# Kernel optimization log

Measured on AMD Instinct MI355X. Metric: run time of the kernel, lower is better.

Reference implementation:

```python
import jax, jax.numpy as jnp
import numpy as np


def setup_inputs() -> dict:
    key = jax.random.key(0)
    k1, k2 = jax.random.split(key)
    B, N, D, F = 4, 50000, 64, 100000
    verts = jax.random.normal(k1, (B, N, D), dtype=jnp.float32)
    faces = jax.random.randint(k2, (B, F, 3), 0, N, dtype=jnp.int64)
    return {"verts": verts, "faces": faces}


def reference(verts, faces):
    # verts: [B, N, D], faces: [B, F, L] int indices into N
    B, N, D = verts.shape
    Ldeg = faces.shape[-1]
    # flatten batch into one block-diagonal graph, as the torch module does
    offset = (jnp.arange(B, dtype=faces.dtype) * N)[:, None, None]
    f = (faces + offset).reshape(-1, Ldeg)          # [B*F, L]
    row = f.reshape(-1)                              # f[:, 0..L-1]
    col = jnp.roll(f, -1, axis=1).reshape(-1)        # f[:, 1..L-1, 0]
    # L = L + L.T -> edges in both directions (duplicates accumulate)
    src = jnp.concatenate([row, col])
    dst = jnp.concatenate([col, row])
    Vf = verts.reshape(-1, D)                        # [B*N, D]
    # off-diagonal: -sum_j V_j over incident half-edges (with multiplicity)
    neigh = jax.ops.segment_sum(Vf[dst], src, num_segments=B * N)
    # Lii = degree (count of incident half-edges)
    deg = jax.ops.segment_sum(jnp.ones_like(src, dtype=verts.dtype), src,
                              num_segments=B * N)    # [B*N]
    # x = (Lii * V_i - sum_j V_j) / (Lii + eps)
    x = (deg[:, None] * Vf - neigh) / (deg[:, None] + 1e-12)
    return x.reshape(B, N, D)
```

## Files before the change

### kernel.cpp

```cpp
#include <hip/hip_runtime.h>
#include <hip/hip_fp16.h>

constexpr int Bc = 4;
constexpr int Nc = 50000;
constexpr int Dc = 64;
constexpr int Fc = 100000;
constexpr int BN = Bc * Nc;
constexpr int NFACES = Bc * Fc;
constexpr int NINC = NFACES * 3;
constexpr int CAP_E = 31;

constexpr int BINV_SH = 8;
constexpr int NBINS   = (BN + 255) / 256;
constexpr int BINCAP  = 2048;
constexpr int BIN3B   = 256;
constexpr int FPB     = (NFACES + BIN3B - 1) / BIN3B;
constexpr int CONVB   = (BN * Dc / 8) / 256;
constexpr unsigned int SENT = (unsigned)Nc | ((unsigned)Nc << 16);

constexpr size_t A_VH    = 0;
constexpr size_t A_ENT   = 25600512;
constexpr size_t A_BCUR  = A_ENT + (size_t)NBINS * BINCAP * 8;
constexpr size_t A3_NEED = A_BCUR + (size_t)NBINS * 32 * 4;

__global__ __launch_bounds__(256) void bin_conv(
        const float* __restrict__ verts,
        const int*   __restrict__ faces,
        __half* __restrict__ vh,
        int*   __restrict__ bincur,
        uint2* __restrict__ entries) {
    __shared__ unsigned int sfaces[FPB * 3];
    __shared__ int scnt[NBINS];
    __shared__ int sbase[NBINS];

    if ((int)blockIdx.x < BIN3B) {
        int blk = blockIdx.x, t = threadIdx.x;
        int f0g = blk * FPB;
        int nf  = NFACES - f0g; if (nf > FPB) nf = FPB;

        for (int i = t; i < nf * 3; i += 256) sfaces[i] = (unsigned int)faces[f0g * 3 + i];
        for (int i = t; i < NBINS; i += 256) scnt[i] = 0;
        __syncthreads();

        for (int f = t; f < nf; f += 256) {
            int base = ((f0g + f) / Fc) * Nc;
            int g0 = (int)sfaces[3*f+0] + base;
            int g1 = (int)sfaces[3*f+1] + base;
            int g2 = (int)sfaces[3*f+2] + base;
            atomicAdd(&scnt[g0 >> BINV_SH], 1);
            atomicAdd(&scnt[g1 >> BINV_SH], 1);
            atomicAdd(&scnt[g2 >> BINV_SH], 1);
        }
        __syncthreads();

        for (int i = t; i < NBINS; i += 256) {
            int c = scnt[i];
            sbase[i] = (c > 0) ? atomicAdd(&bincur[i * 32], c) : 0;
            scnt[i] = 0;
        }
        __syncthreads();

        for (int f = t; f < nf; f += 256) {
            unsigned int u0 = sfaces[3*f+0];
            unsigned int u1 = sfaces[3*f+1];
            unsigned int u2 = sfaces[3*f+2];
            int base = ((f0g + f) / Fc) * Nc;
            int g0 = (int)u0 + base, g1 = (int)u1 + base, g2 = (int)u2 + base;
            int b0 = g0 >> BINV_SH, b1 = g1 >> BINV_SH, b2 = g2 >> BINV_SH;
            int p0 = sbase[b0] + atomicAdd(&scnt[b0], 1);
            if (p0 < BINCAP) entries[(size_t)b0 * BINCAP + p0] = make_uint2((unsigned)g0, u1 | (u2 << 16));
            int p1 = sbase[b1] + atomicAdd(&scnt[b1], 1);
            if (p1 < BINCAP) entries[(size_t)b1 * BINCAP + p1] = make_uint2((unsigned)g1, u0 | (u2 << 16));
            int p2 = sbase[b2] + atomicAdd(&scnt[b2], 1);
            if (p2 < BINCAP) entries[(size_t)b2 * BINCAP + p2] = make_uint2((unsigned)g2, u0 | (u1 << 16));
        }
    } else if ((int)blockIdx.x < BIN3B + CONVB) {
        long idx = ((long)(blockIdx.x - BIN3B) * 256 + threadIdx.x) * 8;
        int  v   = (int)(idx >> 6);
        int  b   = v / Nc;
        float4 a = *(const float4*)(verts + idx);
        float4 bb = *(const float4*)(verts + idx + 4);
        __half h[8];
        h[0] = __float2half(a.x);  h[1] = __float2half(a.y);
        h[2] = __float2half(a.z);  h[3] = __float2half(a.w);
        h[4] = __float2half(bb.x); h[5] = __float2half(bb.y);
        h[6] = __float2half(bb.z); h[7] = __float2half(bb.w);
        *(uint4*)(vh + idx + (long)b * 64) = *(const uint4*)h;
    } else {
        int t = threadIdx.x;
        if (t < 128) {
            int b = t >> 5, w = t & 31;
            ((unsigned int*)vh)[(long)(b * (Nc + 1) + Nc) * 32 + w] = 0u;
        }
    }
}

__global__ __launch_bounds__(256) void bucket_gather(
        const __half* __restrict__ vh,
        const uint2*  __restrict__ entries,
        const int*    __restrict__ bincur,
        float* __restrict__ out) {
    __shared__ unsigned int scnt[256];
    __shared__ unsigned int sent[256 * 32];

    int bin = blockIdx.x, t = threadIdx.x;
    scnt[t] = 0;
    for (int i = t; i < 256 * 32; i += 256) sent[i] = SENT;
    __syncthreads();

    int total = bincur[bin * 32];
    if (total > BINCAP) total = BINCAP;
    const uint2* e = entries + (size_t)bin * BINCAP;
    int v0 = bin << BINV_SH;
    for (int i = t; i < total; i += 256) {
        uint2 en = e[i];
        int vl = (int)en.x - v0;
        unsigned int r = atomicAdd(&scnt[vl], 1);
        if (r < (unsigned)CAP_E) sent[(vl << 5) + r] = en.y;
    }
    __syncthreads();

    int lane = t & 63, wv = t >> 6;
    int half = lane >> 5, j = lane & 31;
    const __half2* vh2 = (const __half2*)vh;
    int nrec = BN - v0; if (nrec > 256) nrec = 256;

    for (int pair = wv; pair * 2 < nrec; pair += 4) {
        int vl = pair * 2 + half;
        int v  = v0 + vl;
        int c  = (int)scnt[vl]; if (c > CAP_E) c = CAP_E;
        int cother = __shfl(c, lane ^ 32);
        int cmax = c > cother ? c : cother;
        int b = v / Nc;
        int base2 = b * (Nc + 1);

        float2 own = __half22float2(vh2[(v + b) * 32 + j]);

        const unsigned int* se = &sent[vl << 5];
        float accx = 0.f, accy = 0.f;
        for (int i = 0; i < cmax; i += 4) {
            unsigned int p0 = se[i];
            unsigned int p1 = se[i + 1];
            unsigned int p2 = se[i + 2];
            unsigned int p3 = se[i + 3];
            int r0 = (base2 + (int)(p0 & 0xFFFFu)) * 32 + j;
            int r1 = (base2 + (int)(p0 >> 16))     * 32 + j;
            int r2 = (base2 + (int)(p1 & 0xFFFFu)) * 32 + j;
            int r3 = (base2 + (int)(p1 >> 16))     * 32 + j;
            int r4 = (base2 + (int)(p2 & 0xFFFFu)) * 32 + j;
            int r5 = (base2 + (int)(p2 >> 16))     * 32 + j;
            int r6 = (base2 + (int)(p3 & 0xFFFFu)) * 32 + j;
            int r7 = (base2 + (int)(p3 >> 16))     * 32 + j;
            float2 f0 = __half22float2(vh2[r0]);
            float2 f1 = __half22float2(vh2[r1]);
            float2 f2 = __half22float2(vh2[r2]);
            float2 f3 = __half22float2(vh2[r3]);
            float2 f4 = __half22float2(vh2[r4]);
            float2 f5 = __half22float2(vh2[r5]);
            float2 f6 = __half22float2(vh2[r6]);
            float2 f7 = __half22float2(vh2[r7]);
            accx += (f0.x + f1.x) + (f2.x + f3.x) + (f4.x + f5.x) + (f6.x + f7.x);
            accy += (f0.y + f1.y) + (f2.y + f3.y) + (f4.y + f5.y) + (f6.y + f7.y);
        }

        float deg = 2.0f * (float)c;
        float den = deg + 1e-12f;
        float2 r;
        r.x = (deg * own.x - accx) / den;
        r.y = (deg * own.y - accy) / den;
        ((float2*)out)[(long)v * 32 + j] = r;
    }
}

constexpr size_t B_VH   = 0;
constexpr size_t B_REC  = 25600000;
constexpr size_t B_NEED = 51200000;

__global__ __launch_bounds__(256) void conv_fill(
        const float* __restrict__ verts,
        const int*   __restrict__ faces,
        __half* __restrict__ vh,
        unsigned int* __restrict__ rec) {
    constexpr int FILLB = (NFACES + 255) / 256;
    if ((int)blockIdx.x < FILLB) {
        int f = blockIdx.x * 256 + threadIdx.x;
        if (f >= NFACES) return;
        int base = (f / Fc) * Nc;
        unsigned int u0 = (unsigned int)faces[3*f+0];
        unsigned int u1 = (unsigned int)faces[3*f+1];
        unsigned int u2 = (unsigned int)faces[3*f+2];
        unsigned int* r0 = rec + (long)((int)u0 + base) * 32;
        unsigned int* r1 = rec + (long)((int)u1 + base) * 32;
        unsigned int* r2 = rec + (long)((int)u2 + base) * 32;
        int s0 = atomicAdd((int*)r0, 1);
        if (s0 < CAP_E) r0[1 + s0] = u1 | (u2 << 16);
        int s1 = atomicAdd((int*)r1, 1);
        if (s1 < CAP_E) r1[1 + s1] = u0 | (u2 << 16);
        int s2 = atomicAdd((int*)r2, 1);
        if (s2 < CAP_E) r2[1 + s2] = u0 | (u1 << 16);
    } else {
        long idx = ((long)(blockIdx.x - FILLB) * 256 + threadIdx.x) * 8;
        float4 a = *(const float4*)(verts + idx);
        float4 b = *(const float4*)(verts + idx + 4);
        __half h[8];
        h[0] = __float2half(a.x); h[1] = __float2half(a.y);
        h[2] = __float2half(a.z); h[3] = __float2half(a.w);
        h[4] = __float2half(b.x); h[5] = __float2half(b.y);
        h[6] = __float2half(b.z); h[7] = __float2half(b.w);
        *(uint4*)(vh + idx) = *(const uint4*)h;
    }
}

__global__ __launch_bounds__(256) void gather2(
        const float*  __restrict__ verts,
        const __half* __restrict__ vh,
        const unsigned int* __restrict__ rec,
        float* __restrict__ out) {
    int gtid = blockIdx.x * 256 + threadIdx.x;
    int w    = gtid >> 6;
    int lane = threadIdx.x & 63;
    int half = lane >> 5;
    int j    = lane & 31;
    int v    = 2 * w + half;
    int h32  = half << 5;

    unsigned int rw = rec[(long)w * 64 + lane];
    int c = __shfl((int)rw, h32);
    if (c > CAP_E) c = CAP_E;
    int cother = __shfl(c, lane ^ 32);
    int cmax = c > cother ? c : cother;

    int base = (v / Nc) * Nc;
    const __half2* vh2 = (const __half2*)vh;
    float2 own = ((const float2*)verts)[(long)v * 32 + j];

    float accx = 0.f, accy = 0.f;
    for (int i = 0; i < cmax; i += 2) {
        unsigned int p0 = (unsigned int)__shfl((int)rw, h32 + 1 + i);
        unsigned int p1 = (unsigned int)__shfl((int)rw, h32 + 2 + i);
        float m0 = (i < c) ? 1.f : 0.f;
        float m1 = (i + 1 < c) ? 1.f : 0.f;
        unsigned int q0 = (i < c) ? p0 : 0u;
        unsigned int q1 = (i + 1 < c) ? p1 : 0u;
        long r0 = (long)(base + (int)(q0 & 0xFFFFu)) * 32 + j;
        long r1 = (long)(base + (int)(q0 >> 16))     * 32 + j;
        long r2 = (long)(base + (int)(q1 & 0xFFFFu)) * 32 + j;
        long r3 = (long)(base + (int)(q1 >> 16))     * 32 + j;
        float2 f0 = __half22float2(vh2[r0]);
        float2 f1 = __half22float2(vh2[r1]);
        float2 f2 = __half22float2(vh2[r2]);
        float2 f3 = __half22float2(vh2[r3]);
        accx += m0 * (f0.x + f1.x) + m1 * (f2.x + f3.x);
        accy += m0 * (f0.y + f1.y) + m1 * (f2.y + f3.y);
    }

    float deg = 2.0f * (float)c;
    float den = deg + 1e-12f;
    float2 r;
    r.x = (deg * own.x - accx) / den;
    r.y = (deg * own.y - accy) / den;
    ((float2*)out)[(long)v * 32 + j] = r;
}

constexpr int SCAN_ELEMS = 1024;
constexpr int NSCAN = (BN + SCAN_ELEMS - 1) / SCAN_ELEMS;
constexpr size_t WS_COUNTS  = 0;
constexpr size_t WS_OFFSETS = 800000;
constexpr size_t WS_CURSORS = 1600000;
constexpr size_t WS_BSUMS   = 2400000;
constexpr size_t WS_BBASE   = 2401024;
constexpr size_t WS_ENTRIES = 2402048;
constexpr size_t WS_NEEDED  = WS_ENTRIES + (size_t)NINC * 8;

__global__ __launch_bounds__(256) void count_kernel(
        const int* __restrict__ faces, int* __restrict__ counts) {
    int f = blockIdx.x * blockDim.x + threadIdx.x;
    if (f >= NFACES) return;
    int base = (f / Fc) * Nc;
    atomicAdd(&counts[faces[3*f+0] + base], 1);
    atomicAdd(&counts[faces[3*f+1] + base], 1);
    atomicAdd(&counts[faces[3*f+2] + base], 1);
}

__global__ __launch_bounds__(256) void scanA(
        const int* __restrict__ counts, int* __restrict__ bsums) {
    __shared__ int s[256];
    int t = threadIdx.x, b = blockIdx.x;
    int idx = b * SCAN_ELEMS + t * 4;
    int v = 0;
    if (idx + 4 <= BN) {
        int4 c = *(const int4*)(counts + idx);
        v = c.x + c.y + c.z + c.w;
    }
    s[t] = v; __syncthreads();
    for (int o = 128; o > 0; o >>= 1) {
        if (t < o) s[t] += s[t + o];
        __syncthreads();
    }
    if (t == 0) bsums[b] = s[0];
}

__global__ __launch_bounds__(256) void scanB(
        const int* __restrict__ bsums, int* __restrict__ bbase) {
    __shared__ int s[256];
    int t = threadIdx.x;
    int x = (t < NSCAN) ? bsums[t] : 0;
    s[t] = x; __syncthreads();
    for (int o = 1; o < 256; o <<= 1) {
        int v = (t >= o) ? s[t - o] : 0;
        __syncthreads();
        s[t] += v;
        __syncthreads();
    }
    bbase[t] = s[t] - x;
}

__global__ __launch_bounds__(256) void scanC(
        const int* __restrict__ counts, const int* __restrict__ bbase,
        int* __restrict__ offsets) {
    __shared__ int s[256];
    int t = threadIdx.x, b = blockIdx.x;
    int idx = b * SCAN_ELEMS + t * 4;
    int4 c = make_int4(0, 0, 0, 0);
    bool ok = (idx + 4 <= BN);
    if (ok) c = *(const int4*)(counts + idx);
    int tsum = c.x + c.y + c.z + c.w;
    s[t] = tsum; __syncthreads();
    for (int o = 1; o < 256; o <<= 1) {
        int v = (t >= o) ? s[t - o] : 0;
        __syncthreads();
        s[t] += v;
        __syncthreads();
    }
    int tbase = bbase[b] + s[t] - tsum;
    if (ok) {
        int4 o4;
        o4.x = tbase;
        o4.y = tbase + c.x;
        o4.z = tbase + c.x + c.y;
        o4.w = tbase + c.x + c.y + c.z;
        *(int4*)(offsets + idx) = o4;
    }
}

__global__ __launch_bounds__(256) void fill_kernel(
        const int* __restrict__ faces,
        const int* __restrict__ offsets,
        int* __restrict__ cursors,
        int2* __restrict__ entries) {
    int f = blockIdx.x * blockDim.x + threadIdx.x;
    if (f >= NFACES) return;
    int base = (f / Fc) * Nc;
    int v0 = faces[3*f+0] + base;
    int v1 = faces[3*f+1] + base;
    int v2 = faces[3*f+2] + base;
    int p0 = offsets[v0] + atomicAdd(&cursors[v0], 1);
    entries[p0] = make_int2(v1, v2);
    int p1 = offsets[v1] + atomicAdd(&cursors[v1], 1);
    entries[p1] = make_int2(v0, v2);
    int p2 = offsets[v2] + atomicAdd(&cursors[v2], 1);
    entries[p2] = make_int2(v0, v1);
}

__global__ __launch_bounds__(256) void gather_kernel(
        const float* __restrict__ verts,
        const int* __restrict__ counts,
        const int* __restrict__ offsets,
        const int2* __restrict__ entries,
        float* __restrict__ out) {
    int v    = (int)((blockIdx.x * blockDim.x + threadIdx.x) >> 6);
    int lane = threadIdx.x & 63;
    if (v >= BN) return;
    int c = counts[v];
    const int2* e = entries + offsets[v];
    float acc = 0.f;
    int i = 0;
    for (; i + 2 <= c; i += 2) {
        int2 a = e[i];
        int2 b = e[i + 1];
        acc += verts[(long)a.x * Dc + lane] + verts[(long)a.y * Dc + lane]
             + verts[(long)b.x * Dc + lane] + verts[(long)b.y * Dc + lane];
    }
    if (i < c) {
        int2 a = e[i];
        acc += verts[(long)a.x * Dc + lane] + verts[(long)a.y * Dc + lane];
    }
    float deg = 2.0f * (float)c;
    float own = verts[(long)v * Dc + lane];
    out[(long)v * Dc + lane] = (deg * own - acc) / (deg + 1e-12f);
}

extern "C" void kernel_launch(void* const* d_in, const int* in_sizes, int n_in,
                              void* d_out, int out_size, void* d_ws, size_t ws_size,
                              hipStream_t stream) {
    const float* verts = (const float*)d_in[0];
    const int*   faces = (const int*)d_in[1];
    float* out = (float*)d_out;
    char*  ws  = (char*)d_ws;

    if (ws_size >= A3_NEED) {
        __half*       vh      = (__half*)(ws + A_VH);
        uint2*        entries = (uint2*)(ws + A_ENT);
        int*          bincur  = (int*)(ws + A_BCUR);

        hipMemsetAsync(bincur, 0, (size_t)NBINS * 32 * sizeof(int), stream);
        bin_conv<<<BIN3B + CONVB + 1, 256, 0, stream>>>(verts, faces, vh, bincur, entries);
        bucket_gather<<<NBINS, 256, 0, stream>>>(vh, entries, bincur, out);
    } else if (ws_size >= B_NEED) {
        __half*       vh  = (__half*)(ws + B_VH);
        unsigned int* rec = (unsigned int*)(ws + B_REC);
        hipMemsetAsync(rec, 0, (size_t)BN * 32 * sizeof(unsigned int), stream);
        conv_fill<<<(NFACES + 255) / 256 + CONVB, 256, 0, stream>>>(verts, faces, vh, rec);
        gather2<<<BN * 32 / 256, 256, 0, stream>>>(verts, vh, rec, out);
    } else if (ws_size >= WS_NEEDED) {
        int*  counts  = (int*)(ws + WS_COUNTS);
        int*  offsets = (int*)(ws + WS_OFFSETS);
        int*  cursors = (int*)(ws + WS_CURSORS);
        int*  bsums   = (int*)(ws + WS_BSUMS);
        int*  bbase   = (int*)(ws + WS_BBASE);
        int2* entries = (int2*)(ws + WS_ENTRIES);

        hipMemsetAsync(counts,  0, (size_t)BN * sizeof(int), stream);
        hipMemsetAsync(cursors, 0, (size_t)BN * sizeof(int), stream);
        int fb = (NFACES + 255) / 256;
        count_kernel<<<fb, 256, 0, stream>>>(faces, counts);
        scanA<<<NSCAN, 256, 0, stream>>>(counts, bsums);
        scanB<<<1, 256, 0, stream>>>(bsums, bbase);
        scanC<<<NSCAN, 256, 0, stream>>>(counts, bbase, offsets);
        fill_kernel<<<fb, 256, 0, stream>>>(faces, offsets, cursors, entries);
        int gb = (BN * 64 + 255) / 256;
        gather_kernel<<<gb, 256, 0, stream>>>(verts, counts, offsets, entries, out);
    }
}
```

Before: 168.0 us.

## Remap gather so each wave handles one vertex with four-way neighbor parallelism

Reworks the bucket_gather inner loop so a 64-lane wave processes one vertex. Four 16-lane groups each fetch a different neighbor row with 8-byte loads, and partial sums are then reduced across groups with xor shuffles. This replaces the two-vertices-per-wave scheme that padded to the longer neighbor list with 4-byte loads. It also vectorizes the shared-memory sentinel fill, writes float4 outputs and multiplies by a reciprocal instead of dividing. The cost is shuffle reductions and idle lanes during the final write, which only group 0 performs.

```diff
diff --git a/kernel.cpp b/kernel.cpp
--- a/kernel.cpp
+++ b/kernel.cpp
@@ -105,7 +105,11 @@
 
     int bin = blockIdx.x, t = threadIdx.x;
     scnt[t] = 0;
-    for (int i = t; i < 256 * 32; i += 256) sent[i] = SENT;
+    {
+        uint4* s4 = (uint4*)sent;
+        uint4 sv = make_uint4(SENT, SENT, SENT, SENT);
+        for (int i = t; i < 256 * 32 / 4; i += 256) s4[i] = sv;
+    }
     __syncthreads();
 
     int total = bincur[bin * 32];
@@ -121,54 +125,53 @@
     __syncthreads();
 
     int lane = t & 63, wv = t >> 6;
-    int half = lane >> 5, j = lane & 31;
-    const __half2* vh2 = (const __half2*)vh;
+    int g    = lane >> 4;
+    int j    = lane & 15;
+    int esel = g >> 1;
+    int hsel = g & 1;
     int nrec = BN - v0; if (nrec > 256) nrec = 256;
 
-    for (int pair = wv; pair * 2 < nrec; pair += 4) {
-        int vl = pair * 2 + half;
-        int v  = v0 + vl;
-        int c  = (int)scnt[vl]; if (c > CAP_E) c = CAP_E;
-        int cother = __shfl(c, lane ^ 32);
-        int cmax = c > cother ? c : cother;
+    const __half* vj = vh + 4 * j;
+
+    for (int vl = wv; vl < nrec; vl += 4) {
+        int v = v0 + vl;
+        int c = (int)scnt[vl]; if (c > CAP_E) c = CAP_E;
         int b = v / Nc;
         int base2 = b * (Nc + 1);
 
-        float2 own = __half22float2(vh2[(v + b) * 32 + j]);
+        float2 o01 = make_float2(0.f, 0.f), o23 = make_float2(0.f, 0.f);
+        if (g == 0) {
+            uint2 ow = *(const uint2*)(vh + (((size_t)(v + b)) << 6) + 4 * j);
+            o01 = __half22float2(*(const __half2*)&ow.x);
+            o23 = __half22float2(*(const __half2*)&ow.y);
+        }
 
         const unsigned int* se = &sent[vl << 5];
-        float accx = 0.f, accy = 0.f;
-        for (int i = 0; i < cmax; i += 4) {
-            unsigned int p0 = se[i];
-            unsigned int p1 = se[i + 1];
-            unsigned int p2 = se[i + 2];
-            unsigned int p3 = se[i + 3];
-            int r0 = (base2 + (int)(p0 & 0xFFFFu)) * 32 + j;
-            int r1 = (base2 + (int)(p0 >> 16))     * 32 + j;
-            int r2 = (base2 + (int)(p1 & 0xFFFFu)) * 32 + j;
-            int r3 = (base2 + (int)(p1 >> 16))     * 32 + j;
-            int r4 = (base2 + (int)(p2 & 0xFFFFu)) * 32 + j;
-            int r5 = (base2 + (int)(p2 >> 16))     * 32 + j;
-            int r6 = (base2 + (int)(p3 & 0xFFFFu)) * 32 + j;
-            int r7 = (base2 + (int)(p3 >> 16))     * 32 + j;
-            float2 f0 = __half22float2(vh2[r0]);
-            float2 f1 = __half22float2(vh2[r1]);
-            float2 f2 = __half22float2(vh2[r2]);
-            float2 f3 = __half22float2(vh2[r3]);
-            float2 f4 = __half22float2(vh2[r4]);
-            float2 f5 = __half22float2(vh2[r5]);
-            float2 f6 = __half22float2(vh2[r6]);
-            float2 f7 = __half22float2(vh2[r7]);
-            accx += (f0.x + f1.x) + (f2.x + f3.x) + (f4.x + f5.x) + (f6.x + f7.x);
-            accy += (f0.y + f1.y) + (f2.y + f3.y) + (f4.y + f5.y) + (f6.y + f7.y);
-        }
-
-        float deg = 2.0f * (float)c;
-        float den = deg + 1e-12f;
-        float2 r;
-        r.x = (deg * own.x - accx) / den;
-        r.y = (deg * own.y - accy) / den;
-        ((float2*)out)[(long)v * 32 + j] = r;
+        float a0 = 0.f, a1 = 0.f, a2 = 0.f, a3 = 0.f;
+        for (int i = 0; i < c; i += 2) {
+            unsigned int w = se[i + esel];
+            int nb = hsel ? (int)(w >> 16) : (int)(w & 0xFFFFu);
+            uint2 d = *(const uint2*)(vj + (((size_t)(base2 + nb)) << 6));
+            float2 f01 = __half22float2(*(const __half2*)&d.x);
+            float2 f23 = __half22float2(*(const __half2*)&d.y);
+            a0 += f01.x; a1 += f01.y; a2 += f23.x; a3 += f23.y;
+        }
+
+        a0 += __shfl_xor(a0, 16); a1 += __shfl_xor(a1, 16);
+        a2 += __shfl_xor(a2, 16); a3 += __shfl_xor(a3, 16);
+        a0 += __shfl_xor(a0, 32); a1 += __shfl_xor(a1, 32);
+        a2 += __shfl_xor(a2, 32); a3 += __shfl_xor(a3, 32);
+
+        if (g == 0) {
+            float deg = 2.0f * (float)c;
+            float inv = 1.0f / (deg + 1e-12f);
+            float4 r;
+            r.x = (deg * o01.x - a0) * inv;
+            r.y = (deg * o01.y - a1) * inv;
+            r.z = (deg * o23.x - a2) * inv;
+            r.w = (deg * o23.y - a3) * inv;
+            *(float4*)(out + (((size_t)v) << 6) + 4 * j) = r;
+        }
     }
 }
 
```

Result: slower. 227.0 us (+35.1%).
